# Performance work log

Hardware: AMD Instinct MI355X
Metric: run time of the kernel (lower is better)

The kernel has to match this reference:

```python
import jax, jax.numpy as jnp
import numpy as np

B, T, L, F = 32, 512, 16, 128   # utterances, max frames, frame-spec width, specgram_height
H = 128                          # hidden_size1 == hidden_size2
C = 61                           # TIMIT phoneme count


def _p(key, shape, scale):
    return jax.random.normal(key, shape, jnp.float32) * scale


def setup_inputs() -> dict:
    key = jax.random.key(0)
    ks = jax.random.split(key, 32)
    s = 1.0 / np.sqrt(H)
    inp = {}
    inp["x"] = jax.random.normal(ks[0], (B, T, L, F), jnp.float32)
    inp["lengths"] = jax.random.randint(ks[1], (B,), T // 2, T + 1, jnp.int32)
    i = 2
    # rnn1: tanh-RNN, 2 layers, bidirectional (layer0 in=F, layer1 in=2H); dir axis 0
    for name, din in (("r1l0", F), ("r1l1", 2 * H)):
        inp[name + "_Wih"] = _p(ks[i], (2, H, din), s); i += 1
        inp[name + "_Whh"] = _p(ks[i], (2, H, H), s); i += 1
        inp[name + "_bih"] = _p(ks[i], (2, H), s); i += 1
        inp[name + "_bhh"] = _p(ks[i], (2, H), s); i += 1
    # rnn2: GRU, 2 layers, bidirectional (in=2H for both layers); gates packed r,z,n
    for name in ("g0", "g1"):
        inp[name + "_Wih"] = _p(ks[i], (2, 3 * H, 2 * H), s); i += 1
        inp[name + "_Whh"] = _p(ks[i], (2, 3 * H, H), s); i += 1
        inp[name + "_bih"] = _p(ks[i], (2, 3 * H), s); i += 1
        inp[name + "_bhh"] = _p(ks[i], (2, 3 * H), s); i += 1
    inp["fc_W"] = _p(ks[i], (C, 2 * H), s); i += 1
    inp["fc_b"] = _p(ks[i], (C,), s)
    return inp


def _rnn_bidir(x, Wih, Whh, bih, bhh):
    # x: (N, S, din) -> (N, S, 2H); PyTorch nn.RNN(tanh), bidirectional
    outs = []
    for d in range(2):
        xw = jnp.einsum('bli,hi->blh', x, Wih[d]) + bih[d]
        W, b = Whh[d], bhh[d]
        def step(h, xt):
            h = jnp.tanh(xt + h @ W.T + b)
            return h, h
        h0 = jnp.zeros((x.shape[0], W.shape[0]), x.dtype)
        _, ys = jax.lax.scan(step, h0, jnp.swapaxes(xw, 0, 1), reverse=(d == 1))
        outs.append(jnp.swapaxes(ys, 0, 1))
    return jnp.concatenate(outs, -1)


def _gru_bidir(x, Wih, Whh, bih, bhh):
    # x: (N, S, din) -> (N, S, 2H); PyTorch nn.GRU, bidirectional
    outs = []
    for d in range(2):
        xw = jnp.einsum('bli,hi->blh', x, Wih[d]) + bih[d]  # (N, S, 3H)
        W, b = Whh[d], bhh[d]
        def step(h, xt):
            g = h @ W.T + b
            xr, xz, xn = jnp.split(xt, 3, -1)
            gr, gz, gn = jnp.split(g, 3, -1)
            r = jax.nn.sigmoid(xr + gr)
            z = jax.nn.sigmoid(xz + gz)
            n = jnp.tanh(xn + r * gn)
            h = (1.0 - z) * n + z * h
            return h, h
        h0 = jnp.zeros((x.shape[0], W.shape[1]), x.dtype)
        _, ys = jax.lax.scan(step, h0, jnp.swapaxes(xw, 0, 1), reverse=(d == 1))
        outs.append(jnp.swapaxes(ys, 0, 1))
    return jnp.concatenate(outs, -1)


def reference(x, lengths,
              r1l0_Wih, r1l0_Whh, r1l0_bih, r1l0_bhh,
              r1l1_Wih, r1l1_Whh, r1l1_bih, r1l1_bhh,
              g0_Wih, g0_Whh, g0_bih, g0_bhh,
              g1_Wih, g1_Whh, g1_bih, g1_bhh,
              fc_W, fc_b):
    b, t, l, f = x.shape
    # per-sample rnn1 loop == one batched pass over all B*T frames (eval mode: no dropout)
    o = _rnn_bidir(x.reshape(b * t, l, f), r1l0_Wih, r1l0_Whh, r1l0_bih, r1l0_bhh)
    o = _rnn_bidir(o, r1l1_Wih, r1l1_Whh, r1l1_bih, r1l1_bhh)
    o = o[:, -1, :].reshape(b, t, 2 * H)       # last inner timestep per frame
    o = _gru_bidir(o, g0_Wih, g0_Whh, g0_bih, g0_bhh)
    o = _gru_bidir(o, g1_Wih, g1_Whh, g1_bih, g1_bhh)
    logits = o @ fc_W.T + fc_b                  # (B, T, C)
    mask = jnp.arange(t)[None, :] < lengths[:, None]
    # ragged scatter: concat first lengths[i] timesteps of each sample
    return logits.reshape(b * t, -1)[mask.reshape(-1)]
```

## Files before the change

### kernel.cpp

```cpp
#include <hip/hip_runtime.h>
#include <hip/hip_bf16.h>

#define B_ 32
#define T_ 512
#define L_ 16
#define F_ 128
#define H_ 128
#define C_ 61
#define NF_ (B_*T_)
#define CH_ 4096

typedef unsigned int u32;
typedef unsigned short u16;
typedef __attribute__((ext_vector_type(8))) short s16x8;
typedef __attribute__((ext_vector_type(4))) float f32x4;

__device__ __forceinline__ float bflo(u32 v){ return __uint_as_float(v << 16); }
__device__ __forceinline__ float bfhi(u32 v){ return __uint_as_float(v & 0xffff0000u); }
__device__ __forceinline__ u16 f2bf(float f){
  u32 u = __float_as_uint(f);
  u += 0x7fffu + ((u >> 16) & 1u);
  return (u16)(u >> 16);
}
__device__ __forceinline__ u32 pack2(float a, float b){
  return (u32)f2bf(a) | ((u32)f2bf(b) << 16);
}
__device__ __forceinline__ u32 cvt_pk_bf16(float a, float b){
  u32 d;
  asm("v_cvt_pk_bf16_f32 %0, %1, %2" : "=v"(d) : "v"(a), "v"(b));
  return d;
}
__device__ __forceinline__ float fast_tanh(float x){
  float e = __expf(2.f*x);
  return 1.f - 2.f*__builtin_amdgcn_rcpf(e + 1.f);
}
__device__ __forceinline__ float fast_sigmoid(float x){
  return __builtin_amdgcn_rcpf(1.f + __expf(-x));
}
__device__ __forceinline__ f32x4 mfma16(s16x8 a, s16x8 b, f32x4 c){
  return __builtin_amdgcn_mfma_f32_16x16x32_bf16(a, b, c, 0, 0, 0);
}
__device__ __forceinline__ void lds_barrier(){
  asm volatile("s_waitcnt lgkmcnt(0)\n\ts_barrier" ::: "memory");
}
__device__ __forceinline__ s16x8 packfrag(const float* p){
  const float4 a = *(const float4*)p;
  const float4 b = *(const float4*)(p+4);
  union { s16x8 v; u32 w[4]; } f;
  f.w[0]=pack2(a.x,a.y); f.w[1]=pack2(a.z,a.w);
  f.w[2]=pack2(b.x,b.y); f.w[3]=pack2(b.z,b.w);
  return f.v;
}

__global__ __launch_bounds__(256) void l0_mfma(
    const float* __restrict__ x,
    const float* __restrict__ Wih,
    const float* __restrict__ Whh,
    const float* __restrict__ bih,
    const float* __restrict__ bhh,
    u16* __restrict__ out)
{
  __shared__ __align__(16) u16 Hb[2][16][136];
  __shared__ __align__(16) u16 Xb[2][16][136];
  const int t = threadIdx.x;
  const int lane = t & 63, wv = t >> 6;
  const int l15 = lane & 15, kg = lane >> 4;
  const int dir = blockIdx.y;
  const int f0 = blockIdx.x * 16;
  s16x8 wih[2][4], whh[2][4];
  {
    const float* Wid = Wih + dir*16384;
    const float* Whd = Whh + dir*16384;
    #pragma unroll
    for (int nt = 0; nt < 2; nt++){
      const int u = wv*32 + nt*16 + l15;
      #pragma unroll
      for (int kc = 0; kc < 4; kc++){
        const int k = kc*32 + kg*8;
        wih[nt][kc] = packfrag(&Wid[u*128 + k]);
        whh[nt][kc] = packfrag(&Whd[u*128 + k]);
      }
    }
  }
  const float bv0 = bih[dir*128 + wv*32 + l15]      + bhh[dir*128 + wv*32 + l15];
  const float bv1 = bih[dir*128 + wv*32 + 16 + l15] + bhh[dir*128 + wv*32 + 16 + l15];
  const f32x4 bs0 = {bv0,bv0,bv0,bv0}, bs1 = {bv1,bv1,bv1,bv1};
  const int sr = t >> 4, sc8 = (t & 15) * 8;
  for (int idx = t; idx < 272; idx += 256)
    ((uint4*)&Hb[0][0][0])[idx] = make_uint4(0,0,0,0);
  {
    const int s0 = dir ? 15 : 0;
    const float4* xp = (const float4*)&x[(size_t)(f0+sr)*2048 + s0*128 + sc8];
    const float4 v0 = xp[0], v1 = xp[1];
    *(uint4*)&Xb[0][sr][sc8] = make_uint4(pack2(v0.x,v0.y),pack2(v0.z,v0.w),
                                          pack2(v1.x,v1.y),pack2(v1.z,v1.w));
  }
  lds_barrier();
  int cur = 0;
  for (int st = 0; st < 16; st++){
    const int s = dir ? (15-st) : st;
    float4 p0,p1;
    if (st < 15){
      const int sn = dir ? (14-st) : (st+1);
      const float4* xp = (const float4*)&x[(size_t)(f0+sr)*2048 + sn*128 + sc8];
      p0 = xp[0]; p1 = xp[1];
    }
    f32x4 acc0 = bs0, acc1 = bs1;
    #pragma unroll
    for (int kc = 0; kc < 4; kc++){
      const int ko = kc*32 + kg*8;
      const s16x8 ax = *(const s16x8*)&Xb[cur][l15][ko];
      const s16x8 ah = *(const s16x8*)&Hb[cur][l15][ko];
      acc0 = mfma16(ax, wih[0][kc], acc0);
      acc1 = mfma16(ax, wih[1][kc], acc1);
      acc0 = mfma16(ah, whh[0][kc], acc0);
      acc1 = mfma16(ah, whh[1][kc], acc1);
    }
    const int u0 = wv*32 + l15, u1 = wv*32 + 16 + l15;
    u16* op = out + (size_t)f0*4096 + s*256 + dir*128;
    #pragma unroll
    for (int r = 0; r < 4; r++){
      const int m = kg*4 + r;
      const u16 h0 = f2bf(fast_tanh(acc0[r]));
      const u16 h1 = f2bf(fast_tanh(acc1[r]));
      Hb[cur^1][m][u0] = h0;
      Hb[cur^1][m][u1] = h1;
      op[(size_t)m*4096 + u0] = h0;
      op[(size_t)m*4096 + u1] = h1;
    }
    if (st < 15){
      *(uint4*)&Xb[cur^1][sr][sc8] = make_uint4(pack2(p0.x,p0.y),pack2(p0.z,p0.w),
                                                pack2(p1.x,p1.y),pack2(p1.z,p1.w));
    }
    lds_barrier();
    cur ^= 1;
  }
}

__global__ __launch_bounds__(256) void l1f_mfma(
    const u16* __restrict__ U,
    const float* __restrict__ Wih,
    const float* __restrict__ Whh,
    const float* __restrict__ bih,
    const float* __restrict__ bhh,
    u16* __restrict__ out)
{
  __shared__ __align__(16) u16 Hb[2][16][136];
  __shared__ __align__(16) u16 Xb[2][16][264];
  const int t = threadIdx.x;
  const int lane = t & 63, wv = t >> 6;
  const int l15 = lane & 15, kg = lane >> 4;
  const int f0 = blockIdx.x * 16;
  s16x8 wih[2][8], whh[2][4];
  {
    #pragma unroll
    for (int nt = 0; nt < 2; nt++){
      const int u = wv*32 + nt*16 + l15;
      #pragma unroll
      for (int kc = 0; kc < 8; kc++)
        wih[nt][kc] = packfrag(&Wih[u*256 + kc*32 + kg*8]);
      #pragma unroll
      for (int kc = 0; kc < 4; kc++)
        whh[nt][kc] = packfrag(&Whh[u*128 + kc*32 + kg*8]);
    }
  }
  const float bv0 = bih[wv*32 + l15]      + bhh[wv*32 + l15];
  const float bv1 = bih[wv*32 + 16 + l15] + bhh[wv*32 + 16 + l15];
  const f32x4 bs0 = {bv0,bv0,bv0,bv0}, bs1 = {bv1,bv1,bv1,bv1};
  const int sr = t >> 4, scu = (t & 15) * 16;
  for (int idx = t; idx < 272; idx += 256)
    ((uint4*)&Hb[0][0][0])[idx] = make_uint4(0,0,0,0);
  {
    const uint4* up = (const uint4*)&U[(size_t)(f0+sr)*4096 + scu];
    uint4 c0 = up[0], c1 = up[1];
    *(uint4*)&Xb[0][sr][scu]   = c0;
    *(uint4*)&Xb[0][sr][scu+8] = c1;
  }
  lds_barrier();
  int cur = 0;
  for (int st = 0; st < 16; st++){
    uint4 c0,c1;
    if (st < 15){
      const uint4* up = (const uint4*)&U[(size_t)(f0+sr)*4096 + (st+1)*256 + scu];
      c0 = up[0]; c1 = up[1];
    }
    f32x4 acc0 = bs0, acc1 = bs1;
    #pragma unroll
    for (int kc = 0; kc < 8; kc++){
      const s16x8 ax = *(const s16x8*)&Xb[cur][l15][kc*32 + kg*8];
      acc0 = mfma16(ax, wih[0][kc], acc0);
      acc1 = mfma16(ax, wih[1][kc], acc1);
    }
    #pragma unroll
    for (int kc = 0; kc < 4; kc++){
      const s16x8 ah = *(const s16x8*)&Hb[cur][l15][kc*32 + kg*8];
      acc0 = mfma16(ah, whh[0][kc], acc0);
      acc1 = mfma16(ah, whh[1][kc], acc1);
    }
    const int u0 = wv*32 + l15, u1 = wv*32 + 16 + l15;
    #pragma unroll
    for (int r = 0; r < 4; r++){
      const int m = kg*4 + r;
      const u16 h0 = f2bf(fast_tanh(acc0[r]));
      const u16 h1 = f2bf(fast_tanh(acc1[r]));
      Hb[cur^1][m][u0] = h0;
      Hb[cur^1][m][u1] = h1;
      if (st == 15){
        out[(size_t)(f0+m)*256 + u0] = h0;
        out[(size_t)(f0+m)*256 + u1] = h1;
      }
    }
    if (st < 15){
      *(uint4*)&Xb[cur^1][sr][scu]   = c0;
      *(uint4*)&Xb[cur^1][sr][scu+8] = c1;
    }
    lds_barrier();
    cur ^= 1;
  }
}

__global__ __launch_bounds__(256) void mfma_gemm(
    const u16* __restrict__ A, int lda,
    const u16* __restrict__ Wb, int K,
    const float* __restrict__ bias,
    float* __restrict__ Cf, u16* __restrict__ Cb, int ldc, int act)
{
  const int t = threadIdx.x;
  const int lane = t & 63, wv = t >> 6;
  const int l15 = lane & 15, kg = lane >> 4;
  const int n0 = blockIdx.x * 32;
  const int m0 = blockIdx.y * 64 + wv*16;
  const u16* Ap = A + (size_t)(m0 + l15)*lda + kg*8;
  const u16* W0 = Wb + (size_t)(n0 + l15)*K + kg*8;
  const u16* W1 = Wb + (size_t)(n0 + 16 + l15)*K + kg*8;
  f32x4 acc0 = {0.f,0.f,0.f,0.f}, acc1 = acc0;
  #pragma unroll 4
  for (int kc = 0; kc < K/32; kc++){
    const s16x8 a  = *(const s16x8*)(Ap + kc*32);
    const s16x8 b0 = *(const s16x8*)(W0 + kc*32);
    const s16x8 b1 = *(const s16x8*)(W1 + kc*32);
    acc0 = mfma16(a, b0, acc0);
    acc1 = mfma16(a, b1, acc1);
  }
  const int col0 = n0 + l15, col1 = n0 + 16 + l15;
  const float bv0 = bias[col0], bv1 = bias[col1];
  #pragma unroll
  for (int r = 0; r < 4; r++){
    const int row = m0 + kg*4 + r;
    float v0 = acc0[r] + bv0, v1 = acc1[r] + bv1;
    if (act){ v0 = fast_tanh(v0); v1 = fast_tanh(v1); }
    if (Cf){
      Cf[(size_t)row*ldc + col0] = v0;
      Cf[(size_t)row*ldc + col1] = v1;
    } else {
      Cb[(size_t)row*ldc + col0] = f2bf(v0);
      Cb[(size_t)row*ldc + col1] = f2bf(v1);
    }
  }
}

__global__ __launch_bounds__(256) void gemm_xw(
    const u16* __restrict__ A, int lda,
    const u16* __restrict__ Wb, int K,
    const float* __restrict__ bih, const float* __restrict__ bhhp,
    float* __restrict__ xwT)
{
  const int t = threadIdx.x;
  const int lane = t & 63, wv = t >> 6;
  const int l15 = lane & 15, kg = lane >> 4;
  const int n0 = blockIdx.x * 32;
  const int m0 = blockIdx.y * 64 + wv*16;
  const u16* Ap = A + (size_t)(m0 + l15)*lda + kg*8;
  const u16* W0 = Wb + (size_t)(n0 + l15)*K + kg*8;
  const u16* W1 = Wb + (size_t)(n0 + 16 + l15)*K + kg*8;
  f32x4 acc0 = {0.f,0.f,0.f,0.f}, acc1 = acc0;
  #pragma unroll 4
  for (int kc = 0; kc < K/32; kc++){
    const s16x8 a  = *(const s16x8*)(Ap + kc*32);
    const s16x8 b0 = *(const s16x8*)(W0 + kc*32);
    const s16x8 b1 = *(const s16x8*)(W1 + kc*32);
    acc0 = mfma16(a, b0, acc0);
    acc1 = mfma16(a, b1, acc1);
  }
  const int col0 = n0 + l15, col1 = n0 + 16 + l15;
  const int row0 = m0 + kg*4;
  const int b = row0 >> 9, tt0 = row0 & 511;
  const int half = b >> 4, bl = b & 15;
  float bv0 = bih[col0], bv1 = bih[col1];
  {
    const int c0 = col0 >= 384 ? col0-384 : col0;
    const int c1 = col1 >= 384 ? col1-384 : col1;
    if ((c0 >> 7) < 2) bv0 += bhhp[col0];
    if ((c1 >> 7) < 2) bv1 += bhhp[col1];
  }
  size_t i0, i1;
  {
    const int d0 = col0 >= 384 ? 1 : 0;
    const int c  = col0 - d0*384;
    const int g = c >> 7, cu = c & 127;
    i0 = (((size_t)d0*512 + tt0)*2 + half)*6144
         + (size_t)(((cu>>4)*4 + ((cu>>2)&3))*16 + bl)*12 + g*4 + (cu&3);
  }
  {
    const int d1 = col1 >= 384 ? 1 : 0;
    const int c  = col1 - d1*384;
    const int g = c >> 7, cu = c & 127;
    i1 = (((size_t)d1*512 + tt0)*2 + half)*6144
         + (size_t)(((cu>>4)*4 + ((cu>>2)&3))*16 + bl)*12 + g*4 + (cu&3);
  }
  #pragma unroll
  for (int r = 0; r < 4; r++){
    xwT[i0 + (size_t)r*12288] = acc0[r] + bv0;
    xwT[i1 + (size_t)r*12288] = acc1[r] + bv1;
  }
}

__global__ __launch_bounds__(256) void prep_kernel(
    const float* __restrict__ g0W, const float* __restrict__ g1W,
    const float* __restrict__ r1Wih,
    const float* __restrict__ r1bih, const float* __restrict__ r1bhh,
    u16* __restrict__ g0o, u16* __restrict__ g1o, u16* __restrict__ r1o,
    float* __restrict__ bo)
{
  const int i = blockIdx.x*256 + threadIdx.x;
  if (i < 196608){ g0o[i] = f2bf(g0W[i]); g1o[i] = f2bf(g1W[i]); }
  if (i < 32768)   r1o[i] = f2bf(r1Wih[32768 + i]);
  if (i < 128)     bo[i]  = r1bih[128+i] + r1bhh[128+i];
}

__global__ __launch_bounds__(512, 1) void gru_mfma(
    const float* __restrict__ xwT,
    const float* __restrict__ Whh,
    const float* __restrict__ bhh,
    u16* __restrict__ hout)
{
  __shared__ __align__(16) u16 h_lds[2][16][136];
  const int t = threadIdx.x;
  const int lane = t & 63, wv = t >> 6;
  const int l15 = lane & 15, kg = lane >> 4;
  const int dir = blockIdx.x & 1, half = blockIdx.x >> 1;
  s16x8 wa[3][4];
  {
    const float* Wd = Whh + (size_t)dir*49152;
    #pragma unroll
    for (int g = 0; g < 3; g++)
      #pragma unroll
      for (int kc = 0; kc < 4; kc++)
        wa[g][kc] = packfrag(&Wd[(size_t)(g*128 + wv*16 + l15)*128
                                 + kc*32 + kg*8]);
  }
  const f32x4 bhn = *(const f32x4*)&bhh[dir*384 + 256 + wv*16 + kg*4];
  if (t < 272) ((uint4*)h_lds)[t] = make_uint4(0,0,0,0);
  f32x4 hreg = {0.f,0.f,0.f,0.f};
  const long tstep = dir ? -49152L : 49152L;
  const char* xb = (const char*)xwT
      + (((size_t)dir*512 + (dir ? 511 : 0))*2 + half)*24576
      + (size_t)(((wv*4 + kg)*16 + l15)*12)*4;
  f32x4 pa[3], pb[3];
  pa[0] = *(const f32x4*)(xb); pa[1] = *(const f32x4*)(xb+16); pa[2] = *(const f32x4*)(xb+32);
  xb += tstep;
  pb[0] = *(const f32x4*)(xb); pb[1] = *(const f32x4*)(xb+16); pb[2] = *(const f32x4*)(xb+32);
  xb += tstep;
  const int hstep = dir ? -256 : 256;
  int hoff = ((half*16 + l15)*512 + (dir ? 511 : 0))*256 + dir*128 + wv*16 + kg*4;
  lds_barrier();
  int cur = 0;

#define GSTEP(PX, DOLOAD)                                                   \
  {                                                                         \
                 \
    f32x4 a0 = PX[0], a1 = PX[1], a2 = bhn;                                 \
    const f32x4 cxn = PX[2];                                                \
    if (DOLOAD){                                                            \
      PX[0] = *(const f32x4*)(xb);                                          \
      PX[1] = *(const f32x4*)(xb+16);                                       \
      PX[2] = *(const f32x4*)(xb+32);                                       \
      xb += tstep;                                                          \
    }                                                                       \
    __builtin_amdgcn_s_setprio(1);                                          \
    _Pragma("unroll")                                                       \
    for (int kc = 0; kc < 4; kc++){                                         \
      const s16x8 hf = *(const s16x8*)&h_lds[cur][l15][kc*32 + kg*8];       \
      a0 = mfma16(wa[0][kc], hf, a0);                                       \
      a1 = mfma16(wa[1][kc], hf, a1);                                       \
      a2 = mfma16(wa[2][kc], hf, a2);                                       \
    }                                                                       \
    __builtin_amdgcn_s_setprio(0);                                          \
    float hn[4];                                                            \
    _Pragma("unroll")                                                       \
    for (int r = 0; r < 4; r++){                                            \
      const float rr = fast_sigmoid(a0[r]);                                 \
      const float zz = fast_sigmoid(a1[r]);                                 \
      const float nn = fast_tanh(fmaf(rr, a2[r], cxn[r]));                  \
      hn[r] = fmaf(zz, hreg[r] - nn, nn);                                   \
      hreg[r] = hn[r];                                                      \
    }                                                                       \
    const uint2 hp = make_uint2(cvt_pk_bf16(hn[0],hn[1]),                   \
                                cvt_pk_bf16(hn[2],hn[3]));                  \
    *(uint2*)&h_lds[cur^1][l15][wv*16 + kg*4] = hp;                         \
    *(uint2*)&hout[hoff] = hp;                                              \
    hoff += hstep;                                                          \
    lds_barrier();                                                          \
    cur ^= 1;                                                               \
  }

  for (int ti = 0; ti < 510; ti += 2){
    GSTEP(pa, 1);
    GSTEP(pb, 1);
  }
  GSTEP(pa, 0);
  GSTEP(pb, 0);
#undef GSTEP
}

__global__ void prefix_kernel(const int* __restrict__ lengths, int* __restrict__ pre){
  if (threadIdx.x == 0 && blockIdx.x == 0){
    int run = 0;
    for (int b = 0; b < 32; b++){ pre[b] = run; run += lengths[b]; }
  }
}

__global__ __launch_bounds__(256) void fc_kernel(
    const u16* __restrict__ A,
    const float* __restrict__ W,
    const float* __restrict__ bias,
    const int* __restrict__ lengths,
    const int* __restrict__ pre,
    float* __restrict__ out)
{
  __shared__ __align__(16) float4 Wl[64][61];
  __shared__ __align__(16) float  Al[64][256];
  const int t = threadIdx.x;
  const int row0 = blockIdx.x * 64;
  for (int idx = t; idx < 61*64; idx += 256){
    int c = idx >> 6, k4 = idx & 63;
    Wl[k4][c] = *(const float4*)&W[(size_t)c*256 + k4*4];
  }
  {
    const u32* A32 = (const u32*)(A + (size_t)row0*256);
    for (int idx = t; idx < 8192; idx += 256){
      u32 v = A32[idx];
      int r = idx >> 7, kp = idx & 127;
      Al[r][2*kp]   = bflo(v);
      Al[r][2*kp+1] = bfhi(v);
    }
  }
  __syncthreads();
  const int c = t & 63;
  const int rbase = t >> 6;
  if (c < 61){
    const float bv = bias[c];
    for (int rr = rbase; rr < 64; rr += 4){
      float s0=0,s1=0,s2=0,s3=0;
      const float4* Ap = (const float4*)&Al[rr][0];
      #pragma unroll
      for (int k4 = 0; k4 < 64; k4++){
        const float4 w = Wl[k4][c];
        const float4 a = Ap[k4];
        s0 = fmaf(w.x, a.x, s0);
        s1 = fmaf(w.y, a.y, s1);
        s2 = fmaf(w.z, a.z, s2);
        s3 = fmaf(w.w, a.w, s3);
      }
      const int n = row0 + rr;
      const int b = n >> 9, tt = n & 511;
      if (tt < lengths[b])
        out[(size_t)(pre[b] + tt)*61 + c] = bv + s0+s1+s2+s3;
    }
  }
}

extern "C" void kernel_launch(void* const* d_in, const int* in_sizes, int n_in,
                              void* d_out, int out_size, void* d_ws, size_t ws_size,
                              hipStream_t stream)
{
  const float* x     = (const float*)d_in[0];
  const int*   lens  = (const int*)d_in[1];
  const float* r0Wih = (const float*)d_in[2];
  const float* r0Whh = (const float*)d_in[3];
  const float* r0bih = (const float*)d_in[4];
  const float* r0bhh = (const float*)d_in[5];
  const float* r1Wih = (const float*)d_in[6];
  const float* r1Whh = (const float*)d_in[7];
  const float* r1bih = (const float*)d_in[8];
  const float* r1bhh = (const float*)d_in[9];
  const float* g0Wih = (const float*)d_in[10];
  const float* g0Whh = (const float*)d_in[11];
  const float* g0bih = (const float*)d_in[12];
  const float* g0bhh = (const float*)d_in[13];
  const float* g1Wih = (const float*)d_in[14];
  const float* g1Whh = (const float*)d_in[15];
  const float* g1bih = (const float*)d_in[16];
  const float* g1bhh = (const float*)d_in[17];
  const float* fcW   = (const float*)d_in[18];
  const float* fcb   = (const float*)d_in[19];
  float* out = (float*)d_out;

  char* ws = (char*)d_ws;
  u16*   l0buf = (u16*)(ws);
  float* xwbuf = (float*)(ws);
  u16*   g0out = (u16*)(ws + 50331648);
  u16*   g0Wb  = (u16*)(ws + 58720256);
  u16*   g1Wb  = (u16*)(ws + 58720256 + 393216);
  u16*   r1Wb  = (u16*)(ws + 58720256 + 786432);
  float* biasb = (float*)(ws + 58720256 + 851968);
  u16*   g1out = (u16*)(ws + 58720256);
  u16*   rnn1  = (u16*)(ws + 67108864);
  int*   pre   = (int*)(ws + 75497472);

  prep_kernel<<<768, 256, 0, stream>>>(g0Wih, g1Wih, r1Wih, r1bih, r1bhh,
                                       g0Wb, g1Wb, r1Wb, biasb);
  for (int c = 0; c < NF_/CH_; c++){
    l0_mfma<<<dim3(CH_/16, 2), 256, 0, stream>>>(
        x + (size_t)c*CH_*2048, r0Wih, r0Whh, r0bih, r0bhh, l0buf);
    l1f_mfma<<<dim3(CH_/16), 256, 0, stream>>>(
        l0buf, r1Wih, r1Whh, r1bih, r1bhh, rnn1 + (size_t)c*CH_*256);
    mfma_gemm<<<dim3(128/32, CH_/64), 256, 0, stream>>>(
        l0buf + 15*256, 4096, r1Wb, 256, biasb,
        (float*)nullptr, rnn1 + (size_t)c*CH_*256 + 128, 256, 1);
  }
  gemm_xw<<<dim3(768/32, NF_/64), 256, 0, stream>>>(
      rnn1, 256, g0Wb, 256, g0bih, g0bhh, xwbuf);
  gru_mfma<<<4, 512, 0, stream>>>(xwbuf, g0Whh, g0bhh, g0out);
  gemm_xw<<<dim3(768/32, NF_/64), 256, 0, stream>>>(
      g0out, 256, g1Wb, 256, g1bih, g1bhh, xwbuf);
  gru_mfma<<<4, 512, 0, stream>>>(xwbuf, g1Whh, g1bhh, g1out);
  prefix_kernel<<<1, 64, 0, stream>>>(lens, pre);
  fc_kernel<<<NF_/64, 256, 0, stream>>>(g1out, fcW, fcb, lens, pre, out);
}
```

Measured before the change: 1.002 ms.

## Process both GRU directions in one workgroup to interleave independent recurrences

The GRU recurrence kernel now handles forward and backward directions in the same block, with 2 blocks instead of 4. Each step interleaves the MFMA chains and gate math of the two independent directions, so their latencies can overlap within one wave. The cost is double the weight registers per thread, which may cause spills given the launch-bounds change. Fewer CUs are used.

```diff
diff --git a/kernel.cpp b/kernel.cpp
--- a/kernel.cpp
+++ b/kernel.cpp
@@ -328,88 +328,112 @@
   if (i < 128)     bo[i]  = r1bih[128+i] + r1bhh[128+i];
 }
 
-__global__ __launch_bounds__(512, 1) void gru_mfma(
+__global__ __launch_bounds__(512, 2) void gru_mfma(
     const float* __restrict__ xwT,
     const float* __restrict__ Whh,
     const float* __restrict__ bhh,
     u16* __restrict__ hout)
 {
-  __shared__ __align__(16) u16 h_lds[2][16][136];
+  __shared__ __align__(16) u16 h_lds[2][2][16][136];
   const int t = threadIdx.x;
   const int lane = t & 63, wv = t >> 6;
   const int l15 = lane & 15, kg = lane >> 4;
-  const int dir = blockIdx.x & 1, half = blockIdx.x >> 1;
-  s16x8 wa[3][4];
-  {
-    const float* Wd = Whh + (size_t)dir*49152;
+  const int half = blockIdx.x;
+  s16x8 wa[2][3][4];
+  #pragma unroll
+  for (int d = 0; d < 2; d++)
     #pragma unroll
     for (int g = 0; g < 3; g++)
       #pragma unroll
       for (int kc = 0; kc < 4; kc++)
-        wa[g][kc] = packfrag(&Wd[(size_t)(g*128 + wv*16 + l15)*128
-                                 + kc*32 + kg*8]);
-  }
-  const f32x4 bhn = *(const f32x4*)&bhh[dir*384 + 256 + wv*16 + kg*4];
-  if (t < 272) ((uint4*)h_lds)[t] = make_uint4(0,0,0,0);
-  f32x4 hreg = {0.f,0.f,0.f,0.f};
-  const long tstep = dir ? -49152L : 49152L;
-  const char* xb = (const char*)xwT
-      + (((size_t)dir*512 + (dir ? 511 : 0))*2 + half)*24576
-      + (size_t)(((wv*4 + kg)*16 + l15)*12)*4;
-  f32x4 pa[3], pb[3];
-  pa[0] = *(const f32x4*)(xb); pa[1] = *(const f32x4*)(xb+16); pa[2] = *(const f32x4*)(xb+32);
-  xb += tstep;
-  pb[0] = *(const f32x4*)(xb); pb[1] = *(const f32x4*)(xb+16); pb[2] = *(const f32x4*)(xb+32);
-  xb += tstep;
-  const int hstep = dir ? -256 : 256;
-  int hoff = ((half*16 + l15)*512 + (dir ? 511 : 0))*256 + dir*128 + wv*16 + kg*4;
+        wa[d][g][kc] = packfrag(&Whh[(size_t)d*49152
+                                     + (size_t)(g*128 + wv*16 + l15)*128
+                                     + kc*32 + kg*8]);
+  f32x4 bhn[2];
+  bhn[0] = *(const f32x4*)&bhh[256 + wv*16 + kg*4];
+  bhn[1] = *(const f32x4*)&bhh[384 + 256 + wv*16 + kg*4];
+  for (int idx = t; idx < 544; idx += 512)
+    ((uint4*)h_lds)[idx] = make_uint4(0,0,0,0);
+  f32x4 hreg0 = {0.f,0.f,0.f,0.f}, hreg1 = hreg0;
+  const size_t laneoff = (size_t)(((wv*4 + kg)*16 + l15)*12)*4;
+  const char* xb0 = (const char*)xwT + (size_t)half*24576 + laneoff;
+  const char* xb1 = (const char*)xwT + ((size_t)(512 + 511)*2 + half)*24576 + laneoff;
+  f32x4 pa0[3], pb0[3], pa1[3], pb1[3];
+  pa0[0] = *(const f32x4*)(xb0); pa0[1] = *(const f32x4*)(xb0+16); pa0[2] = *(const f32x4*)(xb0+32);
+  xb0 += 49152;
+  pb0[0] = *(const f32x4*)(xb0); pb0[1] = *(const f32x4*)(xb0+16); pb0[2] = *(const f32x4*)(xb0+32);
+  xb0 += 49152;
+  pa1[0] = *(const f32x4*)(xb1); pa1[1] = *(const f32x4*)(xb1+16); pa1[2] = *(const f32x4*)(xb1+32);
+  xb1 -= 49152;
+  pb1[0] = *(const f32x4*)(xb1); pb1[1] = *(const f32x4*)(xb1+16); pb1[2] = *(const f32x4*)(xb1+32);
+  xb1 -= 49152;
+  int hoff0 = ((half*16 + l15)*512 + 0)*256 + wv*16 + kg*4;
+  int hoff1 = ((half*16 + l15)*512 + 511)*256 + 128 + wv*16 + kg*4;
   lds_barrier();
   int cur = 0;
 
-#define GSTEP(PX, DOLOAD)                                                   \
+#define GSTEP(PX0, PX1, DOLOAD)                                             \
   {                                                                         \
-                 \
-    f32x4 a0 = PX[0], a1 = PX[1], a2 = bhn;                                 \
-    const f32x4 cxn = PX[2];                                                \
+    f32x4 a00 = PX0[0], a01 = PX0[1], a02 = bhn[0];                         \
+    f32x4 a10 = PX1[0], a11 = PX1[1], a12 = bhn[1];                         \
+    const f32x4 cxn0 = PX0[2], cxn1 = PX1[2];                               \
     if (DOLOAD){                                                            \
-      PX[0] = *(const f32x4*)(xb);                                          \
-      PX[1] = *(const f32x4*)(xb+16);                                       \
-      PX[2] = *(const f32x4*)(xb+32);                                       \
-      xb += tstep;                                                          \
+      PX0[0] = *(const f32x4*)(xb0);                                        \
+      PX0[1] = *(const f32x4*)(xb0+16);                                     \
+      PX0[2] = *(const f32x4*)(xb0+32);                                     \
+      xb0 += 49152;                                                         \
+      PX1[0] = *(const f32x4*)(xb1);                                        \
+      PX1[1] = *(const f32x4*)(xb1+16);                                     \
+      PX1[2] = *(const f32x4*)(xb1+32);                                     \
+      xb1 -= 49152;                                                         \
     }                                                                       \
     __builtin_amdgcn_s_setprio(1);                                          \
     _Pragma("unroll")                                                       \
     for (int kc = 0; kc < 4; kc++){                                         \
-      const s16x8 hf = *(const s16x8*)&h_lds[cur][l15][kc*32 + kg*8];       \
-      a0 = mfma16(wa[0][kc], hf, a0);                                       \
-      a1 = mfma16(wa[1][kc], hf, a1);                                       \
-      a2 = mfma16(wa[2][kc], hf, a2);                                       \
+      const s16x8 hf0 = *(const s16x8*)&h_lds[cur][0][l15][kc*32 + kg*8];   \
+      const s16x8 hf1 = *(const s16x8*)&h_lds[cur][1][l15][kc*32 + kg*8];   \
+      a00 = mfma16(wa[0][0][kc], hf0, a00);                                 \
+      a01 = mfma16(wa[0][1][kc], hf0, a01);                                 \
+      a02 = mfma16(wa[0][2][kc], hf0, a02);                                 \
+      a10 = mfma16(wa[1][0][kc], hf1, a10);                                 \
+      a11 = mfma16(wa[1][1][kc], hf1, a11);                                 \
+      a12 = mfma16(wa[1][2][kc], hf1, a12);                                 \
     }                                                                       \
     __builtin_amdgcn_s_setprio(0);                                          \
-    float hn[4];                                                            \
+    float hn0[4], hn1[4];                                                   \
     _Pragma("unroll")                                                       \
     for (int r = 0; r < 4; r++){                                            \
-      const float rr = fast_sigmoid(a0[r]);                                 \
-      const float zz = fast_sigmoid(a1[r]);                                 \
-      const float nn = fast_tanh(fmaf(rr, a2[r], cxn[r]));                  \
-      hn[r] = fmaf(zz, hreg[r] - nn, nn);                                   \
-      hreg[r] = hn[r];                                                      \
+      const float rr0 = fast_sigmoid(a00[r]);                               \
+      const float rr1 = fast_sigmoid(a10[r]);                               \
+      const float zz0 = fast_sigmoid(a01[r]);                               \
+      const float zz1 = fast_sigmoid(a11[r]);                               \
+      const float nn0 = fast_tanh(fmaf(rr0, a02[r], cxn0[r]));              \
+      const float nn1 = fast_tanh(fmaf(rr1, a12[r], cxn1[r]));              \
+      hn0[r] = fmaf(zz0, hreg0[r] - nn0, nn0);                              \
+      hn1[r] = fmaf(zz1, hreg1[r] - nn1, nn1);                              \
+      hreg0[r] = hn0[r];                                                    \
+      hreg1[r] = hn1[r];                                                    \
     }                                                                       \
-    const uint2 hp = make_uint2(cvt_pk_bf16(hn[0],hn[1]),                   \
-                                cvt_pk_bf16(hn[2],hn[3]));                  \
-    *(uint2*)&h_lds[cur^1][l15][wv*16 + kg*4] = hp;                         \
-    *(uint2*)&hout[hoff] = hp;                                              \
-    hoff += hstep;                                                          \
+    const uint2 hp0 = make_uint2(cvt_pk_bf16(hn0[0],hn0[1]),                \
+                                 cvt_pk_bf16(hn0[2],hn0[3]));               \
+    const uint2 hp1 = make_uint2(cvt_pk_bf16(hn1[0],hn1[1]),                \
+                                 cvt_pk_bf16(hn1[2],hn1[3]));               \
+    *(uint2*)&h_lds[cur^1][0][l15][wv*16 + kg*4] = hp0;                     \
+    *(uint2*)&h_lds[cur^1][1][l15][wv*16 + kg*4] = hp1;                     \
+    *(uint2*)&hout[hoff0] = hp0;                                            \
+    *(uint2*)&hout[hoff1] = hp1;                                            \
+    hoff0 += 256;                                                           \
+    hoff1 -= 256;                                                           \
     lds_barrier();                                                          \
     cur ^= 1;                                                               \
   }
 
   for (int ti = 0; ti < 510; ti += 2){
-    GSTEP(pa, 1);
-    GSTEP(pb, 1);
-  }
-  GSTEP(pa, 0);
-  GSTEP(pb, 0);
+    GSTEP(pa0, pa1, 1);
+    GSTEP(pb0, pb1, 1);
+  }
+  GSTEP(pa0, pa1, 0);
+  GSTEP(pb0, pb1, 0);
 #undef GSTEP
 }
 
@@ -521,10 +545,10 @@
   }
   gemm_xw<<<dim3(768/32, NF_/64), 256, 0, stream>>>(
       rnn1, 256, g0Wb, 256, g0bih, g0bhh, xwbuf);
-  gru_mfma<<<4, 512, 0, stream>>>(xwbuf, g0Whh, g0bhh, g0out);
+  gru_mfma<<<2, 512, 0, stream>>>(xwbuf, g0Whh, g0bhh, g0out);
   gemm_xw<<<dim3(768/32, NF_/64), 256, 0, stream>>>(
       g0out, 256, g1Wb, 256, g1bih, g1bhh, xwbuf);
-  gru_mfma<<<4, 512, 0, stream>>>(xwbuf, g1Whh, g1bhh, g1out);
+  gru_mfma<<<2, 512, 0, stream>>>(xwbuf, g1Whh, g1bhh, g1out);
   prefix_kernel<<<1, 64, 0, stream>>>(lens, pre);
   fc_kernel<<<NF_/64, 256, 0, stream>>>(g1out, fcW, fcb, lens, pre, out);
 }
```

Result: slower. 1.622 ms (+61.9%).

## Fuse layer-1 backward GEMM into l1f, coalesce RNN/GRU output stores, relayout xw

Applied to the files above, without the earlier changes.

The separate mfma_gemm launch for the layer-1 backward direction is folded into the final step of l1f_mfma, which reads the last-step input from LDS and multiplies by r1Wb there. The per-lane scattered bf16 output stores in l0_mfma and gru_mfma become row-contiguous vector stores read back from LDS after the barrier. gemm_xw swaps its MFMA operands and writes a gate-planar [dir*gate][t][b][u] layout with vector f32x4 stores, and the GRU kernel now reads r/z/n from three separate streams. This removes a launch and its extra pass over l0buf and improves store coalescing. In exchange it adds an LDS read per step on the serial GRU critical path and more global load streams.

```diff
diff --git a/kernel.cpp b/kernel.cpp
--- a/kernel.cpp
+++ b/kernel.cpp
@@ -86,6 +86,10 @@
   const float bv1 = bih[dir*128 + wv*32 + 16 + l15] + bhh[dir*128 + wv*32 + 16 + l15];
   const f32x4 bs0 = {bv0,bv0,bv0,bv0}, bs1 = {bv1,bv1,bv1,bv1};
   const int sr = t >> 4, sc8 = (t & 15) * 8;
+  const int ff = t >> 4, u8 = (t & 15) * 8;
+  u16* opbase = out + (size_t)f0*4096 + dir*128;
+  int opoff = ff*4096 + (dir ? 15 : 0)*256 + u8;
+  const int opstep = dir ? -256 : 256;
   for (int idx = t; idx < 272; idx += 256)
     ((uint4*)&Hb[0][0][0])[idx] = make_uint4(0,0,0,0);
   {
@@ -98,7 +102,6 @@
   lds_barrier();
   int cur = 0;
   for (int st = 0; st < 16; st++){
-    const int s = dir ? (15-st) : st;
     float4 p0,p1;
     if (st < 15){
       const int sn = dir ? (14-st) : (st+1);
@@ -117,22 +120,22 @@
       acc1 = mfma16(ah, whh[1][kc], acc1);
     }
     const int u0 = wv*32 + l15, u1 = wv*32 + 16 + l15;
-    u16* op = out + (size_t)f0*4096 + s*256 + dir*128;
     #pragma unroll
     for (int r = 0; r < 4; r++){
       const int m = kg*4 + r;
-      const u16 h0 = f2bf(fast_tanh(acc0[r]));
-      const u16 h1 = f2bf(fast_tanh(acc1[r]));
-      Hb[cur^1][m][u0] = h0;
-      Hb[cur^1][m][u1] = h1;
-      op[(size_t)m*4096 + u0] = h0;
-      op[(size_t)m*4096 + u1] = h1;
+      Hb[cur^1][m][u0] = f2bf(fast_tanh(acc0[r]));
+      Hb[cur^1][m][u1] = f2bf(fast_tanh(acc1[r]));
     }
     if (st < 15){
       *(uint4*)&Xb[cur^1][sr][sc8] = make_uint4(pack2(p0.x,p0.y),pack2(p0.z,p0.w),
                                                 pack2(p1.x,p1.y),pack2(p1.z,p1.w));
     }
     lds_barrier();
+    {
+      const uint4 hv = *(const uint4*)&Hb[cur^1][ff][u8];
+      *(uint4*)&opbase[opoff] = hv;
+      opoff += opstep;
+    }
     cur ^= 1;
   }
 }
@@ -143,6 +146,8 @@
     const float* __restrict__ Whh,
     const float* __restrict__ bih,
     const float* __restrict__ bhh,
+    const u16* __restrict__ r1Wb,
+    const float* __restrict__ biasb,
     u16* __restrict__ out)
 {
   __shared__ __align__(16) u16 Hb[2][16][136];
@@ -210,6 +215,25 @@
         out[(size_t)(f0+m)*256 + u1] = h1;
       }
     }
+    if (st == 15){
+      const float bb0 = biasb[wv*32 + l15];
+      const float bb1 = biasb[wv*32 + 16 + l15];
+      f32x4 ab0 = {bb0,bb0,bb0,bb0}, ab1 = {bb1,bb1,bb1,bb1};
+      #pragma unroll
+      for (int kc = 0; kc < 8; kc++){
+        const s16x8 uf = *(const s16x8*)&Xb[cur][l15][kc*32 + kg*8];
+        const s16x8 w0 = *(const s16x8*)&r1Wb[(size_t)(wv*32 + l15)*256 + kc*32 + kg*8];
+        const s16x8 w1 = *(const s16x8*)&r1Wb[(size_t)(wv*32 + 16 + l15)*256 + kc*32 + kg*8];
+        ab0 = mfma16(uf, w0, ab0);
+        ab1 = mfma16(uf, w1, ab1);
+      }
+      #pragma unroll
+      for (int r = 0; r < 4; r++){
+        const int m = kg*4 + r;
+        out[(size_t)(f0+m)*256 + 128 + wv*32 + l15]      = f2bf(fast_tanh(ab0[r]));
+        out[(size_t)(f0+m)*256 + 128 + wv*32 + 16 + l15] = f2bf(fast_tanh(ab1[r]));
+      }
+    }
     if (st < 15){
       *(uint4*)&Xb[cur^1][sr][scu]   = c0;
       *(uint4*)&Xb[cur^1][sr][scu+8] = c1;
@@ -219,99 +243,46 @@
   }
 }
 
-__global__ __launch_bounds__(256) void mfma_gemm(
-    const u16* __restrict__ A, int lda,
-    const u16* __restrict__ Wb, int K,
-    const float* __restrict__ bias,
-    float* __restrict__ Cf, u16* __restrict__ Cb, int ldc, int act)
+__global__ __launch_bounds__(256) void gemm_xw(
+    const u16* __restrict__ A,
+    const u16* __restrict__ Wb,
+    const float* __restrict__ bih,
+    const float* __restrict__ bhhp,
+    float* __restrict__ xw4)
 {
   const int t = threadIdx.x;
   const int lane = t & 63, wv = t >> 6;
   const int l15 = lane & 15, kg = lane >> 4;
-  const int n0 = blockIdx.x * 32;
-  const int m0 = blockIdx.y * 64 + wv*16;
-  const u16* Ap = A + (size_t)(m0 + l15)*lda + kg*8;
-  const u16* W0 = Wb + (size_t)(n0 + l15)*K + kg*8;
-  const u16* W1 = Wb + (size_t)(n0 + 16 + l15)*K + kg*8;
-  f32x4 acc0 = {0.f,0.f,0.f,0.f}, acc1 = acc0;
-  #pragma unroll 4
-  for (int kc = 0; kc < K/32; kc++){
+  const int ublk = blockIdx.x * 32;
+  const int f0 = blockIdx.y * 64 + wv*16;
+  const u16* Ap = A  + (size_t)(f0 + l15)*256 + kg*8;
+  const u16* W0 = Wb + (size_t)(ublk + l15)*256 + kg*8;
+  const u16* W1 = Wb + (size_t)(ublk + 16 + l15)*256 + kg*8;
+  const int c0 = ublk + kg*4, c1 = c0 + 16;
+  f32x4 acc0 = *(const f32x4*)&bih[c0];
+  f32x4 acc1 = *(const f32x4*)&bih[c1];
+  const int cc0 = c0 >= 384 ? c0 - 384 : c0;
+  const int cc1 = c1 >= 384 ? c1 - 384 : c1;
+  if ((cc0 >> 7) < 2) acc0 += *(const f32x4*)&bhhp[c0];
+  if ((cc1 >> 7) < 2) acc1 += *(const f32x4*)&bhhp[c1];
+  #pragma unroll
+  for (int kc = 0; kc < 8; kc++){
     const s16x8 a  = *(const s16x8*)(Ap + kc*32);
-    const s16x8 b0 = *(const s16x8*)(W0 + kc*32);
-    const s16x8 b1 = *(const s16x8*)(W1 + kc*32);
-    acc0 = mfma16(a, b0, acc0);
-    acc1 = mfma16(a, b1, acc1);
-  }
-  const int col0 = n0 + l15, col1 = n0 + 16 + l15;
-  const float bv0 = bias[col0], bv1 = bias[col1];
-  #pragma unroll
-  for (int r = 0; r < 4; r++){
-    const int row = m0 + kg*4 + r;
-    float v0 = acc0[r] + bv0, v1 = acc1[r] + bv1;
-    if (act){ v0 = fast_tanh(v0); v1 = fast_tanh(v1); }
-    if (Cf){
-      Cf[(size_t)row*ldc + col0] = v0;
-      Cf[(size_t)row*ldc + col1] = v1;
-    } else {
-      Cb[(size_t)row*ldc + col0] = f2bf(v0);
-      Cb[(size_t)row*ldc + col1] = f2bf(v1);
-    }
-  }
-}
-
-__global__ __launch_bounds__(256) void gemm_xw(
-    const u16* __restrict__ A, int lda,
-    const u16* __restrict__ Wb, int K,
-    const float* __restrict__ bih, const float* __restrict__ bhhp,
-    float* __restrict__ xwT)
-{
-  const int t = threadIdx.x;
-  const int lane = t & 63, wv = t >> 6;
-  const int l15 = lane & 15, kg = lane >> 4;
-  const int n0 = blockIdx.x * 32;
-  const int m0 = blockIdx.y * 64 + wv*16;
-  const u16* Ap = A + (size_t)(m0 + l15)*lda + kg*8;
-  const u16* W0 = Wb + (size_t)(n0 + l15)*K + kg*8;
-  const u16* W1 = Wb + (size_t)(n0 + 16 + l15)*K + kg*8;
-  f32x4 acc0 = {0.f,0.f,0.f,0.f}, acc1 = acc0;
-  #pragma unroll 4
-  for (int kc = 0; kc < K/32; kc++){
-    const s16x8 a  = *(const s16x8*)(Ap + kc*32);
-    const s16x8 b0 = *(const s16x8*)(W0 + kc*32);
-    const s16x8 b1 = *(const s16x8*)(W1 + kc*32);
-    acc0 = mfma16(a, b0, acc0);
-    acc1 = mfma16(a, b1, acc1);
-  }
-  const int col0 = n0 + l15, col1 = n0 + 16 + l15;
-  const int row0 = m0 + kg*4;
-  const int b = row0 >> 9, tt0 = row0 & 511;
-  const int half = b >> 4, bl = b & 15;
-  float bv0 = bih[col0], bv1 = bih[col1];
-  {
-    const int c0 = col0 >= 384 ? col0-384 : col0;
-    const int c1 = col1 >= 384 ? col1-384 : col1;
-    if ((c0 >> 7) < 2) bv0 += bhhp[col0];
-    if ((c1 >> 7) < 2) bv1 += bhhp[col1];
-  }
-  size_t i0, i1;
-  {
-    const int d0 = col0 >= 384 ? 1 : 0;
-    const int c  = col0 - d0*384;
-    const int g = c >> 7, cu = c & 127;
-    i0 = (((size_t)d0*512 + tt0)*2 + half)*6144
-         + (size_t)(((cu>>4)*4 + ((cu>>2)&3))*16 + bl)*12 + g*4 + (cu&3);
-  }
-  {
-    const int d1 = col1 >= 384 ? 1 : 0;
-    const int c  = col1 - d1*384;
-    const int g = c >> 7, cu = c & 127;
-    i1 = (((size_t)d1*512 + tt0)*2 + half)*6144
-         + (size_t)(((cu>>4)*4 + ((cu>>2)&3))*16 + bl)*12 + g*4 + (cu&3);
-  }
-  #pragma unroll
-  for (int r = 0; r < 4; r++){
-    xwT[i0 + (size_t)r*12288] = acc0[r] + bv0;
-    xwT[i1 + (size_t)r*12288] = acc1[r] + bv1;
+    const s16x8 w0 = *(const s16x8*)(W0 + kc*32);
+    const s16x8 w1 = *(const s16x8*)(W1 + kc*32);
+    acc0 = mfma16(w0, a, acc0);
+    acc1 = mfma16(w1, a, acc1);
+  }
+  const int f = f0 + l15, b = f >> 9, tt = f & 511;
+  {
+    const int d = c0 >= 384 ? 1 : 0;
+    const int g = cc0 >> 7, u = cc0 & 127;
+    *(f32x4*)&xw4[(((size_t)(d*3+g)*512 + tt)*32 + b)*128 + u] = acc0;
+  }
+  {
+    const int d = c1 >= 384 ? 1 : 0;
+    const int g = cc1 >> 7, u = cc1 & 127;
+    *(f32x4*)&xw4[(((size_t)(d*3+g)*512 + tt)*32 + b)*128 + u] = acc1;
   }
 }
 
@@ -329,7 +300,7 @@
 }
 
 __global__ __launch_bounds__(512, 1) void gru_mfma(
-    const float* __restrict__ xwT,
+    const float* __restrict__ xw4,
     const float* __restrict__ Whh,
     const float* __restrict__ bhh,
     u16* __restrict__ hout)
@@ -352,30 +323,33 @@
   const f32x4 bhn = *(const f32x4*)&bhh[dir*384 + 256 + wv*16 + kg*4];
   if (t < 272) ((uint4*)h_lds)[t] = make_uint4(0,0,0,0);
   f32x4 hreg = {0.f,0.f,0.f,0.f};
-  const long tstep = dir ? -49152L : 49152L;
-  const char* xb = (const char*)xwT
-      + (((size_t)dir*512 + (dir ? 511 : 0))*2 + half)*24576
-      + (size_t)(((wv*4 + kg)*16 + l15)*12)*4;
+  const int tt0 = dir ? 511 : 0;
+  const long tstep = dir ? -16384L : 16384L;
+  const size_t gplane = 512L*32*128*4;
+  const char* xr = (const char*)xw4
+      + ((((size_t)(dir*3)*512 + tt0)*32 + half*16 + l15)*128 + wv*16 + kg*4)*4;
+  const char* xz = xr + gplane;
+  const char* xn = xz + gplane;
   f32x4 pa[3], pb[3];
-  pa[0] = *(const f32x4*)(xb); pa[1] = *(const f32x4*)(xb+16); pa[2] = *(const f32x4*)(xb+32);
-  xb += tstep;
-  pb[0] = *(const f32x4*)(xb); pb[1] = *(const f32x4*)(xb+16); pb[2] = *(const f32x4*)(xb+32);
-  xb += tstep;
-  const int hstep = dir ? -256 : 256;
-  int hoff = ((half*16 + l15)*512 + (dir ? 511 : 0))*256 + dir*128 + wv*16 + kg*4;
+  pa[0] = *(const f32x4*)xr; pa[1] = *(const f32x4*)xz; pa[2] = *(const f32x4*)xn;
+  xr += tstep; xz += tstep; xn += tstep;
+  pb[0] = *(const f32x4*)xr; pb[1] = *(const f32x4*)xz; pb[2] = *(const f32x4*)xn;
+  xr += tstep; xz += tstep; xn += tstep;
+  const int fb = t >> 5, u4 = (t & 31) * 4;
+  int foff = ((half*16 + fb)*512 + tt0)*256 + dir*128 + u4;
+  const int fstep = dir ? -256 : 256;
   lds_barrier();
   int cur = 0;
 
 #define GSTEP(PX, DOLOAD)                                                   \
   {                                                                         \
-                 \
     f32x4 a0 = PX[0], a1 = PX[1], a2 = bhn;                                 \
     const f32x4 cxn = PX[2];                                                \
     if (DOLOAD){                                                            \
-      PX[0] = *(const f32x4*)(xb);                                          \
-      PX[1] = *(const f32x4*)(xb+16);                                       \
-      PX[2] = *(const f32x4*)(xb+32);                                       \
-      xb += tstep;                                                          \
+      PX[0] = *(const f32x4*)xr;                                            \
+      PX[1] = *(const f32x4*)xz;                                            \
+      PX[2] = *(const f32x4*)xn;                                            \
+      xr += tstep; xz += tstep; xn += tstep;                                \
     }                                                                       \
     __builtin_amdgcn_s_setprio(1);                                          \
     _Pragma("unroll")                                                       \
@@ -398,9 +372,12 @@
     const uint2 hp = make_uint2(cvt_pk_bf16(hn[0],hn[1]),                   \
                                 cvt_pk_bf16(hn[2],hn[3]));                  \
     *(uint2*)&h_lds[cur^1][l15][wv*16 + kg*4] = hp;                         \
-    *(uint2*)&hout[hoff] = hp;                                              \
-    hoff += hstep;                                                          \
     lds_barrier();                                                          \
+    {                                                                       \
+      const uint2 hv = *(const uint2*)&h_lds[cur^1][fb][u4];                \
+      *(uint2*)&hout[foff] = hv;                                            \
+      foff += fstep;                                                        \
+    }                                                                       \
     cur ^= 1;                                                               \
   }
 
@@ -514,16 +491,14 @@
     l0_mfma<<<dim3(CH_/16, 2), 256, 0, stream>>>(
         x + (size_t)c*CH_*2048, r0Wih, r0Whh, r0bih, r0bhh, l0buf);
     l1f_mfma<<<dim3(CH_/16), 256, 0, stream>>>(
-        l0buf, r1Wih, r1Whh, r1bih, r1bhh, rnn1 + (size_t)c*CH_*256);
-    mfma_gemm<<<dim3(128/32, CH_/64), 256, 0, stream>>>(
-        l0buf + 15*256, 4096, r1Wb, 256, biasb,
-        (float*)nullptr, rnn1 + (size_t)c*CH_*256 + 128, 256, 1);
-  }
-  gemm_xw<<<dim3(768/32, NF_/64), 256, 0, stream>>>(
-      rnn1, 256, g0Wb, 256, g0bih, g0bhh, xwbuf);
+        l0buf, r1Wih, r1Whh, r1bih, r1bhh, r1Wb, biasb,
+        rnn1 + (size_t)c*CH_*256);
+  }
+  gemm_xw<<<dim3(24, NF_/64), 256, 0, stream>>>(
+      rnn1, g0Wb, g0bih, g0bhh, xwbuf);
   gru_mfma<<<4, 512, 0, stream>>>(xwbuf, g0Whh, g0bhh, g0out);
-  gemm_xw<<<dim3(768/32, NF_/64), 256, 0, stream>>>(
-      g0out, 256, g1Wb, 256, g1bih, g1bhh, xwbuf);
+  gemm_xw<<<dim3(24, NF_/64), 256, 0, stream>>>(
+      g0out, g1Wb, g1bih, g1bhh, xwbuf);
   gru_mfma<<<4, 512, 0, stream>>>(xwbuf, g1Whh, g1bhh, g1out);
   prefix_kernel<<<1, 64, 0, stream>>>(lens, pre);
   fc_kernel<<<NF_/64, 256, 0, stream>>>(g1out, fcW, fcb, lens, pre, out);
```

Result: slower. 1.139 ms (+13.7%).
